# Performance work log

Hardware: AMD Instinct MI355X
Metric: run time of the kernel (lower is better)

Reference implementation:

```python
import jax, jax.numpy as jnp
import numpy as np

N_NODES = 100000
N_EDGES = 1600000
HIDDEN = 128
N_ETYPES = 4
N_STEPS = 4


def setup_inputs() -> dict:
    key = jax.random.key(0)
    ks = jax.random.split(key, 10)
    s = 1.0 / np.sqrt(HIDDEN)
    node_feat = jax.random.normal(ks[0], (N_NODES, HIDDEN), dtype=jnp.float32)
    edge_index = jax.random.randint(ks[1], (2, N_EDGES), 0, N_NODES)
    edge_feat = jax.random.uniform(ks[2], (N_EDGES, N_ETYPES), dtype=jnp.float32)
    # per-edge-type linear layers (DGL GatedGraphConv uses nn.Linear per etype)
    W_edge = jax.random.uniform(ks[3], (N_ETYPES, HIDDEN, HIDDEN), minval=-s, maxval=s, dtype=jnp.float32)
    b_edge = jax.random.uniform(ks[4], (N_ETYPES, HIDDEN), minval=-s, maxval=s, dtype=jnp.float32)
    # GRUCell parameters (torch layout: gates stacked r, z, n)
    W_ih = jax.random.uniform(ks[5], (3 * HIDDEN, HIDDEN), minval=-s, maxval=s, dtype=jnp.float32)
    W_hh = jax.random.uniform(ks[6], (3 * HIDDEN, HIDDEN), minval=-s, maxval=s, dtype=jnp.float32)
    b_ih = jax.random.uniform(ks[7], (3 * HIDDEN,), minval=-s, maxval=s, dtype=jnp.float32)
    b_hh = jax.random.uniform(ks[8], (3 * HIDDEN,), minval=-s, maxval=s, dtype=jnp.float32)
    return {"node_feat": node_feat, "edge_index": edge_index, "edge_feat": edge_feat,
            "W_edge": W_edge, "b_edge": b_edge, "W_ih": W_ih, "W_hh": W_hh,
            "b_ih": b_ih, "b_hh": b_hh}


def _gru_cell(x, h, W_ih, W_hh, b_ih, b_hh):
    gi = x @ W_ih.T + b_ih  # (N, 3D)
    gh = h @ W_hh.T + b_hh
    ir, iz, inn = jnp.split(gi, 3, axis=1)
    hr, hz, hn = jnp.split(gh, 3, axis=1)
    r = jax.nn.sigmoid(ir + hr)
    z = jax.nn.sigmoid(iz + hz)
    n = jnp.tanh(inn + r * hn)
    return (1.0 - z) * n + z * h


def reference(node_feat, edge_index, edge_feat, W_edge, b_edge, W_ih, W_hh, b_ih, b_hh):
    etypes = jnp.argmax(edge_feat, axis=1)          # (E,)
    src, dst = edge_index[0], edge_index[1]
    N = node_feat.shape[0]
    h = node_feat
    for _ in range(N_STEPS):
        # per-etype linear transform of all nodes: (T, N, D)
        trans = jnp.einsum('nd,tod->tno', h, W_edge) + b_edge[:, None, :]
        msg = trans[etypes, src]                    # (E, D) gather by (etype, src)
        a = jax.ops.segment_sum(msg, dst, num_segments=N)  # scatter-add to dst
        h = _gru_cell(a, h, W_ih, W_hh, b_ih, b_hh)
    return h
```

## Files before the change

kernel.cpp:

```cpp
#include <hip/hip_runtime.h>

#define N_NODES 100000
#define N_EDGES 1600000
#define HID 128
#define SCAN_N (N_NODES*4)
#define NB1 ((SCAN_N + 1023) / 1024)
#define ZERO_IDX (N_NODES*4)

#define EB 8192
#define NBLKA ((N_EDGES + EB - 1) / EB)
#define BSH 9
#define NBUCK ((N_NODES + (1<<BSH) - 1) >> BSH)
#define N2 (NBUCK * NBLKA)
#define NB2 ((N2 + 1023) / 1024)

typedef __attribute__((ext_vector_type(8))) short short8;
typedef __attribute__((ext_vector_type(4))) float float4v;
typedef __attribute__((ext_vector_type(4))) int int4v;
typedef __attribute__((ext_vector_type(2))) unsigned int uint2v;
typedef unsigned short ushort_t;
typedef unsigned int uint_t;

__device__ __forceinline__ float bits2f(uint_t u){ union{uint_t u; float f;} x; x.u=u; return x.f; }
__device__ __forceinline__ float b2f(ushort_t u){ return bits2f(((uint_t)u)<<16); }
__device__ __forceinline__ ushort_t f2b(float f){
  union{float f; uint_t u;} x; x.f=f;
  uint_t r = x.u + 0x7fffu + ((x.u>>16)&1u);
  return (ushort_t)(r>>16);
}
__device__ __forceinline__ float fsigm(float x){ return __builtin_amdgcn_rcpf(1.0f + __expf(-x)); }
__device__ __forceinline__ float ftanh(float x){ return 2.0f*__builtin_amdgcn_rcpf(1.0f + __expf(-2.0f*x)) - 1.0f; }
__device__ __forceinline__ float sigm(float x){ return 1.0f/(1.0f+__expf(-x)); }
__device__ __forceinline__ float tanh_f(float x){
  float t=__expf(-2.0f*fabsf(x)); float y=(1.0f-t)/(1.0f+t); return x>=0.f? y : -y;
}
__device__ __forceinline__ int imin(int a, int b){ return a < b ? a : b; }


__global__ void prep_weights(const float* __restrict__ W_edge, const float* __restrict__ W_ih,
                             const float* __restrict__ W_hh, ushort_t* __restrict__ WY,
                             ushort_t* __restrict__ W2f, ushort_t* __restrict__ WYf){
  int i = blockIdx.x*256 + threadIdx.x;
  if (i < 65536){
    WY[i] = f2b(W_edge[i]);
  } else if (i < 65536 + 131072){
    int i2 = i - 65536;
    int tile = i2 >> 9, e9 = i2 & 511;
    int lane = e9 >> 3, e = e9 & 7;
    int kk = tile & 1, kt = (tile >> 1) & 3, j = (tile >> 3) & 7, wn = tile >> 6;
    int lq = lane >> 4, l15 = lane & 15;
    int c = wn*32 + (j&1)*16 + l15;
    int jg = j >> 1;
    int k = kt*64 + (kk*4 + lq)*8 + e;
    float v;
    if (jg < 2)       v = (k < 128) ? W_ih[(jg*128 + c)*128 + k] : W_hh[(jg*128 + c)*128 + (k-128)];
    else if (jg == 2) v = (k < 128) ? W_ih[(256 + c)*128 + k] : 0.0f;
    else              v = (k >= 128) ? W_hh[(256 + c)*128 + (k-128)] : 0.0f;
    W2f[i2] = f2b(v);
  } else if (i < 65536 + 131072 + 65536){
    int i3 = i - 65536 - 131072;
    int tile = i3 >> 9, e9 = i3 & 511;
    int lane = e9 >> 3, e = e9 & 7;
    int kc = tile & 3, j = (tile >> 2) & 7, wn = tile >> 5;
    int lq = lane >> 4, l15 = lane & 15;
    int n = wn*128 + j*16 + l15;
    int k = kc*32 + lq*8 + e;
    WYf[i3] = f2b(W_edge[n*128 + k]);
  }
}

__global__ void edge_pass1(const int* __restrict__ eidx, const float* __restrict__ efeat,
                           int* __restrict__ packed, int* __restrict__ cnt,
                           int* __restrict__ bcntT){
  __shared__ int hist[NBUCK];
  int tid = threadIdx.x, blk = blockIdx.x;
  for (int j = tid; j < NBUCK; j += 512) hist[j] = 0;
  __syncthreads();
  #pragma unroll
  for (int k = 0; k < EB/512; ++k){
    int e = blk*EB + k*512 + tid;
    if (e < N_EDGES){
      int src = eidx[e], dst = eidx[N_EDGES + e];
      float4v f = *(const float4v*)(efeat + (size_t)e*4);
      int t = 0; float b = f[0];
      if (f[1] > b){ b = f[1]; t = 1; }
      if (f[2] > b){ b = f[2]; t = 2; }
      if (f[3] > b){ b = f[3]; t = 3; }
      packed[e] = (src << 2) | t;
      atomicAdd(&cnt[dst*4 + t], 1);
      atomicAdd(&hist[dst >> BSH], 1);
    }
  }
  __syncthreads();
  for (int j = tid; j < NBUCK; j += 512) bcntT[j*NBLKA + blk] = hist[j];
}

__global__ void scan_pass1(const int* __restrict__ src, int* __restrict__ bsum, int n){
  __shared__ int ws[4];
  int tid = threadIdx.x, lane = tid & 63, w = tid >> 6;
  int idx = blockIdx.x*1024 + tid*4;
  int v = 0;
  if (idx + 3 < n){ int4v x = *(const int4v*)(src + idx); v = x[0]+x[1]+x[2]+x[3]; }
  else { for (int k = 0; k < 4; ++k) if (idx + k < n) v += src[idx+k]; }
  for (int d = 32; d; d >>= 1) v += __shfl_down(v, d);
  if (lane == 0) ws[w] = v;
  __syncthreads();
  if (tid == 0) bsum[blockIdx.x] = ws[0]+ws[1]+ws[2]+ws[3];
}

__global__ void scan_pass2(const int* __restrict__ bsum, int* __restrict__ bpre,
                           int* __restrict__ total_out, int nb){
  __shared__ int sh[512];
  int tid = threadIdx.x;
  int v = (tid < nb) ? bsum[tid] : 0;
  sh[tid] = v;
  __syncthreads();
  for (int d = 1; d < 512; d <<= 1){
    int y = (tid >= d) ? sh[tid-d] : 0;
    __syncthreads();
    sh[tid] += y;
    __syncthreads();
  }
  if (tid < nb) bpre[tid] = sh[tid] - v;
  if (tid == 511) *total_out = sh[511];
}

__global__ void scan_pass3(const int* __restrict__ src, const int* __restrict__ bpre,
                           int* __restrict__ off, int n){
  __shared__ int wsum[4];
  int tid = threadIdx.x, lane = tid & 63, w = tid >> 6;
  int idx = blockIdx.x*1024 + tid*4;
  int v0=0,v1=0,v2=0,v3=0;
  if (idx + 3 < n){ int4v x = *(const int4v*)(src + idx); v0=x[0];v1=x[1];v2=x[2];v3=x[3]; }
  else {
    if (idx   < n) v0 = src[idx];
    if (idx+1 < n) v1 = src[idx+1];
    if (idx+2 < n) v2 = src[idx+2];
    if (idx+3 < n) v3 = src[idx+3];
  }
  int ts = v0+v1+v2+v3;
  int sc = ts;
  for (int d = 1; d < 64; d <<= 1){ int y = __shfl_up(sc, d); if (lane >= d) sc += y; }
  if (lane == 63) wsum[w] = sc;
  __syncthreads();
  int wofs = 0;
  for (int k = 0; k < w; ++k) wofs += wsum[k];
  int base = bpre[blockIdx.x] + wofs + sc - ts;
  int e0 = base, e1 = e0+v0, e2 = e1+v1, e3 = e2+v2;
  if (idx   < n) off[idx  ] = e0;
  if (idx+1 < n) off[idx+1] = e1;
  if (idx+2 < n) off[idx+2] = e2;
  if (idx+3 < n) off[idx+3] = e3;
}

__global__ void bucket_scatter(const int* __restrict__ eidx, const int* __restrict__ packed,
                               const int* __restrict__ boffT, int* __restrict__ bucketed){
  __shared__ int cur[NBUCK];
  int tid = threadIdx.x, blk = blockIdx.x;
  for (int j = tid; j < NBUCK; j += 512) cur[j] = boffT[j*NBLKA + blk];
  __syncthreads();
  #pragma unroll
  for (int k = 0; k < EB/512; ++k){
    int e = blk*EB + k*512 + tid;
    if (e < N_EDGES){
      int dst = eidx[N_EDGES + e];
      int pos = atomicAdd(&cur[dst >> BSH], 1);
      bucketed[pos] = ((dst & ((1<<BSH)-1)) << 19) | packed[e];
    }
  }
}

__global__ void bucket_sort(const int* __restrict__ bucketed, const int* __restrict__ boffT,
                            const int* __restrict__ off4, int* __restrict__ sorted){
  __shared__ int cur[(1<<BSH)*4];
  int tid = threadIdx.x, b = blockIdx.x;
  int base = b * ((1<<BSH)*4);
  for (int j = tid; j < (1<<BSH)*4; j += 512)
    cur[j] = off4[imin(base + j, SCAN_N)];
  __syncthreads();
  int s = boffT[b*NBLKA];
  int e = boffT[(b+1)*NBLKA];
  for (int i = s + tid; i < e; i += 512){
    int w = bucketed[i];
    int ci = ((w >> 19) << 2) | (w & 3);
    int pos = atomicAdd(&cur[ci], 1);
    sorted[pos] = w & 0x7FFFF;
  }
}

__global__ void init_h(const float* __restrict__ nf, ushort_t* __restrict__ hB, int n4){
  int i = blockIdx.x*256 + threadIdx.x;
  if (i >= n4) return;
  float4v v = *(const float4v*)(nf + (size_t)i*4);
  uint2v u;
  u[0] = (uint_t)f2b(v[0]) | ((uint_t)f2b(v[1])<<16);
  u[1] = (uint_t)f2b(v[2]) | ((uint_t)f2b(v[3])<<16);
  *(uint2v*)(hB + (size_t)i*4) = u;
}


__launch_bounds__(512, 2)
__global__ void transform_kernel(const ushort_t* __restrict__ hB, const ushort_t* __restrict__ WY,
                                 ushort_t* __restrict__ Y){
  __shared__ ushort_t lA[128*64];
  __shared__ ushort_t lB[512*64];
  int tid = threadIdx.x, w = tid >> 6, lane = tid & 63;
  int wm = w >> 2, wn = w & 3;
  int row0 = blockIdx.x * 128;
  float4v acc[4][8] = {};
  for (int kt = 0; kt < 2; ++kt){
    short8 va[2], vb[8];
    #pragma unroll
    for (int i = 0; i < 2; ++i){
      int cidx = i*512 + tid;
      int r = cidx >> 3, ch = cidx & 7;
      int node = row0 + r; if (node >= N_NODES) node = N_NODES-1;
      va[i] = *reinterpret_cast<const short8*>(hB + (size_t)node*128 + kt*64 + ch*8);
    }
    #pragma unroll
    for (int i = 0; i < 8; ++i){
      int cidx = i*512 + tid;
      int n = cidx >> 3, ch = cidx & 7;
      vb[i] = *reinterpret_cast<const short8*>(WY + (size_t)n*128 + kt*64 + ch*8);
    }
    __syncthreads();
    #pragma unroll
    for (int i = 0; i < 2; ++i){
      int cidx = i*512 + tid;
      int r = cidx >> 3, ch = cidx & 7;
      *reinterpret_cast<short8*>(lA + r*64 + ((ch ^ (r&7))<<3)) = va[i];
    }
    #pragma unroll
    for (int i = 0; i < 8; ++i){
      int cidx = i*512 + tid;
      int n = cidx >> 3, ch = cidx & 7;
      *reinterpret_cast<short8*>(lB + n*64 + ((ch ^ (n&7))<<3)) = vb[i];
    }
    __syncthreads();
    #pragma unroll
    for (int kk = 0; kk < 2; ++kk){
      int lch = kk*4 + (lane>>4);
      short8 af[4], bf[8];
      #pragma unroll
      for (int i = 0; i < 4; ++i){
        int r = wm*64 + i*16 + (lane&15);
        af[i] = *reinterpret_cast<const short8*>(lA + r*64 + ((lch ^ (r&7))<<3));
      }
      #pragma unroll
      for (int j = 0; j < 8; ++j){
        int n = wn*128 + j*16 + (lane&15);
        bf[j] = *reinterpret_cast<const short8*>(lB + n*64 + ((lch ^ (n&7))<<3));
      }
      #pragma unroll
      for (int i = 0; i < 4; ++i)
        #pragma unroll
        for (int j = 0; j < 8; ++j)
          acc[i][j] = __builtin_amdgcn_mfma_f32_16x16x32_bf16(af[i], bf[j], acc[i][j], 0, 0, 0);
    }
    __syncthreads();
  }
  #pragma unroll
  for (int i = 0; i < 4; ++i)
    #pragma unroll
    for (int j = 0; j < 8; ++j)
      #pragma unroll
      for (int q = 0; q < 4; ++q){
        int grow = row0 + wm*64 + i*16 + (lane>>4)*4 + q;
        if (grow >= N_NODES) continue;
        int colc = wn*128 + j*16 + (lane&15);
        Y[(size_t)grow*512 + colc] = f2b(acc[i][j][q]);
      }
}

__global__ void agg_kernel(const int* __restrict__ off4, const int* __restrict__ sorted,
                           const ushort_t* __restrict__ Y, const int* __restrict__ cnt,
                           const float* __restrict__ b_edge, ushort_t* __restrict__ aB){
  int wid = (int)((blockIdx.x * blockDim.x + threadIdx.x) >> 6);
  int lane = threadIdx.x & 63;
  if (wid >= N_NODES) return;
  int s = off4[wid*4], e = off4[wid*4+4];
  int col = lane*2;
  float p0=0,p1=0,q0=0,q1=0,r0=0,r1=0,t0=0,t1=0;
  for (int i = s; i < e; i += 16){
    int vv[16];
    #pragma unroll
    for (int k = 0; k < 16; ++k){
      int j = i + k;
      int sv = sorted[imin(j, e-1)];
      vv[k] = __builtin_amdgcn_readfirstlane(j < e ? sv : ZERO_IDX);
    }
    uint_t hv[16];
    #pragma unroll
    for (int k = 0; k < 16; ++k)
      hv[k] = *(const uint_t*)(Y + (size_t)vv[k]*128 + col);
    #pragma unroll
    for (int k = 0; k < 16; ++k){
      float f0 = bits2f((hv[k] & 0xffffu) << 16);
      float f1 = bits2f(hv[k] & 0xffff0000u);
      if ((k&3)==0){ p0+=f0; p1+=f1; }
      else if ((k&3)==1){ q0+=f0; q1+=f1; }
      else if ((k&3)==2){ r0+=f0; r1+=f1; }
      else { t0+=f0; t1+=f1; }
    }
  }
  float s0 = (p0+q0)+(r0+t0);
  float s1 = (p1+q1)+(r1+t1);
  int4v c4 = *(const int4v*)(cnt + wid*4);
  #pragma unroll
  for (int t = 0; t < 4; ++t){
    float cf = (float)c4[t];
    s0 += cf * b_edge[t*128 + col];
    s1 += cf * b_edge[t*128 + col + 1];
  }
  *(uint_t*)(aB + (size_t)wid*128 + col) = (uint_t)f2b(s0) | ((uint_t)f2b(s1) << 16);
}

__launch_bounds__(512, 4)
__global__ void gru_tr_kernel(const ushort_t* __restrict__ aB, ushort_t* __restrict__ hB,
                              const ushort_t* __restrict__ W2f, const ushort_t* __restrict__ WYf,
                              const float* __restrict__ b_ih, const float* __restrict__ b_hh,
                              float* __restrict__ hF, ushort_t* __restrict__ Y, int last){
  __shared__ ushort_t lA[2][4096];
  __shared__ ushort_t lH[8192];
  int tid = threadIdx.x, w = tid >> 6, lane = tid & 63;
  int wm = w >> 2, wn = w & 3;
  int l15 = lane & 15, lq = lane >> 4;
  int row0 = blockIdx.x * 64;

  int rS = tid >> 3, chS = tid & 7;
  int nodeS = imin(row0 + rS, N_NODES-1);
  size_t aoffS = (size_t)nodeS*128 + chS*8;
  int woS = rS*64 + ((chS ^ (rS&7))<<3);

  *reinterpret_cast<short8*>(&lA[0][woS]) = *reinterpret_cast<const short8*>(aB + aoffS);
  __syncthreads();

  float4v acc[2][8] = {};
  #pragma unroll
  for (int kt = 0; kt < 4; ++kt){
    short8 vn = {};
    if (kt < 3){
      const ushort_t* srcN = (kt+1 < 2) ? aB : hB;
      vn = *reinterpret_cast<const short8*>(srcN + aoffS + ((kt+1)&1)*64);
    }
    bool lo = (kt < 2);
    const ushort_t* lcur = lA[kt&1];
    #pragma unroll
    for (int kk = 0; kk < 2; ++kk){
      int lch = kk*4 + lq;
      short8 af[2];
      #pragma unroll
      for (int i = 0; i < 2; ++i){
        int r = wm*32 + i*16 + l15;
        af[i] = *reinterpret_cast<const short8*>(lcur + r*64 + ((lch ^ (r&7))<<3));
      }
      #pragma unroll
      for (int j = 0; j < 8; ++j){
        if (lo ? (j >= 6) : (j == 4 || j == 5)) continue;
        int tile = ((wn*8 + j)*4 + kt)*2 + kk;
        short8 bf = *reinterpret_cast<const short8*>(W2f + (size_t)tile*512 + lane*8);
        #pragma unroll
        for (int i = 0; i < 2; ++i)
          acc[i][j] = __builtin_amdgcn_mfma_f32_16x16x32_bf16(af[i], bf, acc[i][j], 0, 0, 0);
      }
    }
    if (kt < 3)
      *reinterpret_cast<short8*>(&lA[(kt+1)&1][woS]) = vn;
    __syncthreads();
  }
  #pragma unroll
  for (int i = 0; i < 2; ++i){
    #pragma unroll
    for (int jj = 0; jj < 2; ++jj){
      int c = wn*32 + jj*16 + l15;
      float bir = b_ih[c] + b_hh[c];
      float biz = b_ih[128+c] + b_hh[128+c];
      float bni = b_ih[256+c], bnh = b_hh[256+c];
      int cl = c & 63;
      const ushort_t* lh = lA[c >> 6];
      int ch = c >> 3;
      #pragma unroll
      for (int q = 0; q < 4; ++q){
        int row = wm*32 + i*16 + lq*4 + q;
        float rg = fsigm(acc[i][0+jj][q] + bir);
        float zg = fsigm(acc[i][2+jj][q] + biz);
        float hn = acc[i][6+jj][q] + bnh;
        float nn = ftanh(acc[i][4+jj][q] + bni + rg*hn);
        float h = b2f(lh[row*64 + (((cl>>3) ^ (row&7))<<3) + (cl&7)]);
        float out = (1.0f - zg)*nn + zg*h;
        lH[row*128 + ((ch ^ (row&15))<<3) + (c&7)] = f2b(out);
      }
    }
  }
  __syncthreads();
  #pragma unroll
  for (int p = 0; p < 2; ++p){
    int u = p*512 + tid;
    int row = u >> 4, uc = u & 15;
    int grow = row0 + row;
    if (grow < N_NODES){
      short8 v = *reinterpret_cast<const short8*>(lH + row*128 + ((uc ^ (row&15))<<3));
      *reinterpret_cast<short8*>(hB + (size_t)grow*128 + uc*8) = v;
      if (last){
        float4v f0, f1;
        #pragma unroll
        for (int k = 0; k < 4; ++k) f0[k] = b2f((ushort_t)v[k]);
        #pragma unroll
        for (int k = 0; k < 4; ++k) f1[k] = b2f((ushort_t)v[4+k]);
        *reinterpret_cast<float4v*>(hF + (size_t)grow*128 + uc*8)     = f0;
        *reinterpret_cast<float4v*>(hF + (size_t)grow*128 + uc*8 + 4) = f1;
      }
    }
  }
  if (last) return;
  float4v acc2[2][8] = {};
  #pragma unroll
  for (int kc = 0; kc < 4; ++kc){
    int lchh = kc*4 + lq;
    short8 af[2];
    #pragma unroll
    for (int i = 0; i < 2; ++i){
      int r = wm*32 + i*16 + l15;
      af[i] = *reinterpret_cast<const short8*>(lH + r*128 + ((lchh ^ (r&15))<<3));
    }
    #pragma unroll
    for (int j = 0; j < 8; ++j){
      int tile = (wn*8 + j)*4 + kc;
      short8 bf = *reinterpret_cast<const short8*>(WYf + (size_t)tile*512 + lane*8);
      #pragma unroll
      for (int i = 0; i < 2; ++i)
        acc2[i][j] = __builtin_amdgcn_mfma_f32_16x16x32_bf16(af[i], bf, acc2[i][j], 0, 0, 0);
    }
  }
  #pragma unroll
  for (int i = 0; i < 2; ++i)
    #pragma unroll
    for (int q = 0; q < 4; ++q){
      int grow = row0 + wm*32 + i*16 + lq*4 + q;
      if (grow >= N_NODES) continue;
      #pragma unroll
      for (int j = 0; j < 8; ++j)
        Y[(size_t)grow*512 + wn*128 + j*16 + l15] = f2b(acc2[i][q == 0 ? j : j][q]);
    }
}


extern "C" void kernel_launch(void* const* d_in, const int* in_sizes, int n_in,
                              void* d_out, int out_size, void* d_ws, size_t ws_size,
                              hipStream_t stream) {
  const float* node_feat = (const float*)d_in[0];
  const int*   edge_idx  = (const int*)d_in[1];
  const float* edge_feat = (const float*)d_in[2];
  const float* W_edge    = (const float*)d_in[3];
  const float* b_edge    = (const float*)d_in[4];
  const float* W_ih      = (const float*)d_in[5];
  const float* W_hh      = (const float*)d_in[6];
  const float* b_ih      = (const float*)d_in[7];
  const float* b_hh      = (const float*)d_in[8];
  float* hF = (float*)d_out;

  char* p = (char*)d_ws;
  auto take = [&](size_t bytes) -> char* {
    char* r = p; p += (bytes + 255) & ~(size_t)255; return r;
  };
  ushort_t* WY     = (ushort_t*)take(512*128*2);
  ushort_t* W2f    = (ushort_t*)take(131072*2);
  ushort_t* WYf    = (ushort_t*)take(65536*2);
  int* cnt      = (int*)take((size_t)SCAN_N*4);
  int* off4     = (int*)take((size_t)(SCAN_N+1)*4);
  int* bcntT    = (int*)take((size_t)N2*4);
  int* boffT    = (int*)take((size_t)(N2+1)*4);
  int* bsum     = (int*)take(512*4);
  int* bpre     = (int*)take(512*4);
  int* packed   = (int*)take((size_t)N_EDGES*4);
  int* bucketed = (int*)take((size_t)N_EDGES*4);
  int* sorted   = (int*)take((size_t)N_EDGES*4);
  ushort_t* hB = (ushort_t*)take((size_t)N_NODES*128*2);
  ushort_t* Y  = (ushort_t*)take(((size_t)N_NODES*512 + 256)*2);
  ushort_t* aB = (ushort_t*)take((size_t)N_NODES*128*2);

  hipMemsetAsync(cnt, 0, (size_t)SCAN_N*4, stream);
  hipMemsetAsync(Y + (size_t)N_NODES*512, 0, 256*2, stream);

  prep_weights<<<1024, 256, 0, stream>>>(W_edge, W_ih, W_hh, WY, W2f, WYf);
  edge_pass1<<<NBLKA, 512, 0, stream>>>(edge_idx, edge_feat, packed, cnt, bcntT);
  scan_pass1<<<NB1, 256, 0, stream>>>(cnt, bsum, SCAN_N);
  scan_pass2<<<1, 512, 0, stream>>>(bsum, bpre, off4 + SCAN_N, NB1);
  scan_pass3<<<NB1, 256, 0, stream>>>(cnt, bpre, off4, SCAN_N);
  scan_pass1<<<NB2, 256, 0, stream>>>(bcntT, bsum, N2);
  scan_pass2<<<1, 512, 0, stream>>>(bsum, bpre, boffT + N2, NB2);
  scan_pass3<<<NB2, 256, 0, stream>>>(bcntT, bpre, boffT, N2);
  bucket_scatter<<<NBLKA, 512, 0, stream>>>(edge_idx, packed, boffT, bucketed);
  bucket_sort<<<NBUCK, 512, 0, stream>>>(bucketed, boffT, off4, sorted);
  init_h<<<(N_NODES*32 + 255)/256, 256, 0, stream>>>(node_feat, hB, N_NODES*32);

  int gb = (N_NODES + 127) / 128;
  int gb2 = (N_NODES + 63) / 64;
  transform_kernel<<<gb, 512, 0, stream>>>(hB, WY, Y);
  for (int step = 0; step < 4; ++step){
    agg_kernel<<<(N_NODES+3)/4, 256, 0, stream>>>(off4, sorted, Y, cnt, b_edge, aB);
    gru_tr_kernel<<<gb2, 512, 0, stream>>>(aB, hB, W2f, WYf, b_ih, b_hh, hF, Y, step == 3);
  }
}
```

Baseline: 759.0 us.

## Permute hidden-feature order so MFMA epilogues emit packed vector stores

Hidden features are stored everywhere in a permuted order (pinv) chosen so each lane's MFMA accumulator columns are contiguous. Transform and GRU epilogues can then pack eight outputs with v_cvt_pk_bf16_f32 into one 16-byte store instead of scattered 2-byte stores. Weights, biases and the initial state are permuted once in the prep and init kernels. The cost is that the final fp32 output is un-permuted with strided scalar stores, and init_h now does scattered reads.

```diff
diff --git a/kernel.cpp b/kernel.cpp
--- a/kernel.cpp
+++ b/kernel.cpp
@@ -17,6 +17,7 @@
 typedef __attribute__((ext_vector_type(8))) short short8;
 typedef __attribute__((ext_vector_type(4))) float float4v;
 typedef __attribute__((ext_vector_type(4))) int int4v;
+typedef __attribute__((ext_vector_type(4))) unsigned int uint4v;
 typedef __attribute__((ext_vector_type(2))) unsigned int uint2v;
 typedef unsigned short ushort_t;
 typedef unsigned int uint_t;
@@ -28,21 +29,23 @@
   uint_t r = x.u + 0x7fffu + ((x.u>>16)&1u);
   return (ushort_t)(r>>16);
 }
+__device__ __forceinline__ uint_t cvtpk(float a, float b){
+  uint_t r; asm("v_cvt_pk_bf16_f32 %0, %1, %2" : "=v"(r) : "v"(a), "v"(b)); return r;
+}
 __device__ __forceinline__ float fsigm(float x){ return __builtin_amdgcn_rcpf(1.0f + __expf(-x)); }
 __device__ __forceinline__ float ftanh(float x){ return 2.0f*__builtin_amdgcn_rcpf(1.0f + __expf(-2.0f*x)) - 1.0f; }
-__device__ __forceinline__ float sigm(float x){ return 1.0f/(1.0f+__expf(-x)); }
-__device__ __forceinline__ float tanh_f(float x){
-  float t=__expf(-2.0f*fabsf(x)); float y=(1.0f-t)/(1.0f+t); return x>=0.f? y : -y;
-}
 __device__ __forceinline__ int imin(int a, int b){ return a < b ? a : b; }
+__device__ __forceinline__ int pinv(int p){ return ((p&7)<<4) | (p>>3); }
 
 
 __global__ void prep_weights(const float* __restrict__ W_edge, const float* __restrict__ W_ih,
-                             const float* __restrict__ W_hh, ushort_t* __restrict__ WY,
-                             ushort_t* __restrict__ W2f, ushort_t* __restrict__ WYf){
+                             const float* __restrict__ W_hh, const float* __restrict__ b_edge,
+                             ushort_t* __restrict__ WY, ushort_t* __restrict__ W2f,
+                             ushort_t* __restrict__ WYf, float* __restrict__ bEp){
   int i = blockIdx.x*256 + threadIdx.x;
   if (i < 65536){
-    WY[i] = f2b(W_edge[i]);
+    int g = i >> 7, p = i & 127;
+    WY[i] = f2b(W_edge[g*128 + pinv(p)]);
   } else if (i < 65536 + 131072){
     int i2 = i - 65536;
     int tile = i2 >> 9, e9 = i2 & 511;
@@ -52,10 +55,12 @@
     int c = wn*32 + (j&1)*16 + l15;
     int jg = j >> 1;
     int k = kt*64 + (kk*4 + lq)*8 + e;
+    int d = pinv(k & 127);
+    bool aside = (k < 128);
     float v;
-    if (jg < 2)       v = (k < 128) ? W_ih[(jg*128 + c)*128 + k] : W_hh[(jg*128 + c)*128 + (k-128)];
-    else if (jg == 2) v = (k < 128) ? W_ih[(256 + c)*128 + k] : 0.0f;
-    else              v = (k >= 128) ? W_hh[(256 + c)*128 + (k-128)] : 0.0f;
+    if (jg < 2)       v = aside ? W_ih[(jg*128 + c)*128 + d] : W_hh[(jg*128 + c)*128 + d];
+    else if (jg == 2) v = aside ? W_ih[(256 + c)*128 + d] : 0.0f;
+    else              v = aside ? 0.0f : W_hh[(256 + c)*128 + d];
     W2f[i2] = f2b(v);
   } else if (i < 65536 + 131072 + 65536){
     int i3 = i - 65536 - 131072;
@@ -65,7 +70,11 @@
     int lq = lane >> 4, l15 = lane & 15;
     int n = wn*128 + j*16 + l15;
     int k = kc*32 + lq*8 + e;
-    WYf[i3] = f2b(W_edge[n*128 + k]);
+    WYf[i3] = f2b(W_edge[n*128 + pinv(k)]);
+  } else if (i < 65536 + 131072 + 65536 + 512){
+    int i4 = i - 65536 - 131072 - 65536;
+    int t = i4 >> 7, p = i4 & 127;
+    bEp[i4] = b_edge[t*128 + pinv(p)];
   }
 }
 
@@ -188,14 +197,13 @@
   }
 }
 
-__global__ void init_h(const float* __restrict__ nf, ushort_t* __restrict__ hB, int n4){
+__global__ void init_h(const float* __restrict__ nf, ushort_t* __restrict__ hB, int n){
   int i = blockIdx.x*256 + threadIdx.x;
-  if (i >= n4) return;
-  float4v v = *(const float4v*)(nf + (size_t)i*4);
-  uint2v u;
-  u[0] = (uint_t)f2b(v[0]) | ((uint_t)f2b(v[1])<<16);
-  u[1] = (uint_t)f2b(v[2]) | ((uint_t)f2b(v[3])<<16);
-  *(uint2v*)(hB + (size_t)i*4) = u;
+  if (i >= n) return;
+  int v = i >> 6, pp = (i & 63)*2;
+  float f0 = nf[(size_t)v*128 + pinv(pp)];
+  float f1 = nf[(size_t)v*128 + pinv(pp+1)];
+  *(uint_t*)(hB + (size_t)v*128 + pp) = (uint_t)f2b(f0) | ((uint_t)f2b(f1)<<16);
 }
 
 
@@ -259,22 +267,25 @@
     }
     __syncthreads();
   }
+  int l15 = lane & 15;
   #pragma unroll
   for (int i = 0; i < 4; ++i)
     #pragma unroll
-    for (int j = 0; j < 8; ++j)
-      #pragma unroll
-      for (int q = 0; q < 4; ++q){
-        int grow = row0 + wm*64 + i*16 + (lane>>4)*4 + q;
-        if (grow >= N_NODES) continue;
-        int colc = wn*128 + j*16 + (lane&15);
-        Y[(size_t)grow*512 + colc] = f2b(acc[i][j][q]);
-      }
+    for (int q = 0; q < 4; ++q){
+      int grow = row0 + wm*64 + i*16 + (lane>>4)*4 + q;
+      if (grow >= N_NODES) continue;
+      uint4v u;
+      u[0] = cvtpk(acc[i][0][q], acc[i][1][q]);
+      u[1] = cvtpk(acc[i][2][q], acc[i][3][q]);
+      u[2] = cvtpk(acc[i][4][q], acc[i][5][q]);
+      u[3] = cvtpk(acc[i][6][q], acc[i][7][q]);
+      *reinterpret_cast<uint4v*>(Y + (size_t)grow*512 + wn*128 + l15*8) = u;
+    }
 }
 
 __global__ void agg_kernel(const int* __restrict__ off4, const int* __restrict__ sorted,
                            const ushort_t* __restrict__ Y, const int* __restrict__ cnt,
-                           const float* __restrict__ b_edge, ushort_t* __restrict__ aB){
+                           const float* __restrict__ bEp, ushort_t* __restrict__ aB){
   int wid = (int)((blockIdx.x * blockDim.x + threadIdx.x) >> 6);
   int lane = threadIdx.x & 63;
   if (wid >= N_NODES) return;
@@ -309,8 +320,8 @@
   #pragma unroll
   for (int t = 0; t < 4; ++t){
     float cf = (float)c4[t];
-    s0 += cf * b_edge[t*128 + col];
-    s1 += cf * b_edge[t*128 + col + 1];
+    s0 += cf * bEp[t*128 + col];
+    s1 += cf * bEp[t*128 + col + 1];
   }
   *(uint_t*)(aB + (size_t)wid*128 + col) = (uint_t)f2b(s0) | ((uint_t)f2b(s1) << 16);
 }
@@ -368,27 +379,32 @@
       *reinterpret_cast<short8*>(&lA[(kt+1)&1][woS]) = vn;
     __syncthreads();
   }
-  #pragma unroll
-  for (int i = 0; i < 2; ++i){
-    #pragma unroll
-    for (int jj = 0; jj < 2; ++jj){
-      int c = wn*32 + jj*16 + l15;
-      float bir = b_ih[c] + b_hh[c];
-      float biz = b_ih[128+c] + b_hh[128+c];
-      float bni = b_ih[256+c], bnh = b_hh[256+c];
-      int cl = c & 63;
-      const ushort_t* lh = lA[c >> 6];
-      int ch = c >> 3;
+  {
+    int c0 = wn*32 + l15, c1 = c0 + 16;
+    float bir0 = b_ih[c0] + b_hh[c0],       bir1 = b_ih[c1] + b_hh[c1];
+    float biz0 = b_ih[128+c0] + b_hh[128+c0], biz1 = b_ih[128+c1] + b_hh[128+c1];
+    float bni0 = b_ih[256+c0], bni1 = b_ih[256+c1];
+    float bnh0 = b_hh[256+c0], bnh1 = b_hh[256+c1];
+    int sc = l15*8 + wn*2;
+    const ushort_t* lhh = lA[sc >> 6];
+    int scl = sc & 63;
+    #pragma unroll
+    for (int i = 0; i < 2; ++i){
       #pragma unroll
       for (int q = 0; q < 4; ++q){
         int row = wm*32 + i*16 + lq*4 + q;
-        float rg = fsigm(acc[i][0+jj][q] + bir);
-        float zg = fsigm(acc[i][2+jj][q] + biz);
-        float hn = acc[i][6+jj][q] + bnh;
-        float nn = ftanh(acc[i][4+jj][q] + bni + rg*hn);
-        float h = b2f(lh[row*64 + (((cl>>3) ^ (row&7))<<3) + (cl&7)]);
-        float out = (1.0f - zg)*nn + zg*h;
-        lH[row*128 + ((ch ^ (row&15))<<3) + (c&7)] = f2b(out);
+        uint_t hu = *(const uint_t*)(lhh + row*64 + (((scl>>3) ^ (row&7))<<3) + (scl&7));
+        float h0 = bits2f((hu & 0xffffu) << 16);
+        float h1 = bits2f(hu & 0xffff0000u);
+        float rg0 = fsigm(acc[i][0][q] + bir0);
+        float zg0 = fsigm(acc[i][2][q] + biz0);
+        float nn0 = ftanh(acc[i][4][q] + bni0 + rg0*(acc[i][6][q] + bnh0));
+        float out0 = (1.0f - zg0)*nn0 + zg0*h0;
+        float rg1 = fsigm(acc[i][1][q] + bir1);
+        float zg1 = fsigm(acc[i][3][q] + biz1);
+        float nn1 = ftanh(acc[i][5][q] + bni1 + rg1*(acc[i][7][q] + bnh1));
+        float out1 = (1.0f - zg1)*nn1 + zg1*h1;
+        *(uint_t*)(lH + row*128 + ((l15 ^ (row&15))<<3) + wn*2) = cvtpk(out0, out1);
       }
     }
   }
@@ -402,13 +418,9 @@
       short8 v = *reinterpret_cast<const short8*>(lH + row*128 + ((uc ^ (row&15))<<3));
       *reinterpret_cast<short8*>(hB + (size_t)grow*128 + uc*8) = v;
       if (last){
-        float4v f0, f1;
         #pragma unroll
-        for (int k = 0; k < 4; ++k) f0[k] = b2f((ushort_t)v[k]);
-        #pragma unroll
-        for (int k = 0; k < 4; ++k) f1[k] = b2f((ushort_t)v[4+k]);
-        *reinterpret_cast<float4v*>(hF + (size_t)grow*128 + uc*8)     = f0;
-        *reinterpret_cast<float4v*>(hF + (size_t)grow*128 + uc*8 + 4) = f1;
+        for (int s = 0; s < 8; ++s)
+          hF[(size_t)grow*128 + s*16 + uc] = b2f((ushort_t)v[s]);
       }
     }
   }
@@ -438,9 +450,12 @@
     for (int q = 0; q < 4; ++q){
       int grow = row0 + wm*32 + i*16 + lq*4 + q;
       if (grow >= N_NODES) continue;
-      #pragma unroll
-      for (int j = 0; j < 8; ++j)
-        Y[(size_t)grow*512 + wn*128 + j*16 + l15] = f2b(acc2[i][q == 0 ? j : j][q]);
+      uint4v u;
+      u[0] = cvtpk(acc2[i][0][q], acc2[i][1][q]);
+      u[1] = cvtpk(acc2[i][2][q], acc2[i][3][q]);
+      u[2] = cvtpk(acc2[i][4][q], acc2[i][5][q]);
+      u[3] = cvtpk(acc2[i][6][q], acc2[i][7][q]);
+      *reinterpret_cast<uint4v*>(Y + (size_t)grow*512 + wn*128 + l15*8) = u;
     }
 }
 
@@ -466,6 +481,7 @@
   ushort_t* WY     = (ushort_t*)take(512*128*2);
   ushort_t* W2f    = (ushort_t*)take(131072*2);
   ushort_t* WYf    = (ushort_t*)take(65536*2);
+  float*    bEp    = (float*)take(512*4);
   int* cnt      = (int*)take((size_t)SCAN_N*4);
   int* off4     = (int*)take((size_t)(SCAN_N+1)*4);
   int* bcntT    = (int*)take((size_t)N2*4);
@@ -482,7 +498,7 @@
   hipMemsetAsync(cnt, 0, (size_t)SCAN_N*4, stream);
   hipMemsetAsync(Y + (size_t)N_NODES*512, 0, 256*2, stream);
 
-  prep_weights<<<1024, 256, 0, stream>>>(W_edge, W_ih, W_hh, WY, W2f, WYf);
+  prep_weights<<<1028, 256, 0, stream>>>(W_edge, W_ih, W_hh, b_edge, WY, W2f, WYf, bEp);
   edge_pass1<<<NBLKA, 512, 0, stream>>>(edge_idx, edge_feat, packed, cnt, bcntT);
   scan_pass1<<<NB1, 256, 0, stream>>>(cnt, bsum, SCAN_N);
   scan_pass2<<<1, 512, 0, stream>>>(bsum, bpre, off4 + SCAN_N, NB1);
@@ -492,13 +508,13 @@
   scan_pass3<<<NB2, 256, 0, stream>>>(bcntT, bpre, boffT, N2);
   bucket_scatter<<<NBLKA, 512, 0, stream>>>(edge_idx, packed, boffT, bucketed);
   bucket_sort<<<NBUCK, 512, 0, stream>>>(bucketed, boffT, off4, sorted);
-  init_h<<<(N_NODES*32 + 255)/256, 256, 0, stream>>>(node_feat, hB, N_NODES*32);
+  init_h<<<(N_NODES*64 + 255)/256, 256, 0, stream>>>(node_feat, hB, N_NODES*64);
 
   int gb = (N_NODES + 127) / 128;
   int gb2 = (N_NODES + 63) / 64;
   transform_kernel<<<gb, 512, 0, stream>>>(hB, WY, Y);
   for (int step = 0; step < 4; ++step){
-    agg_kernel<<<(N_NODES+3)/4, 256, 0, stream>>>(off4, sorted, Y, cnt, b_edge, aB);
+    agg_kernel<<<(N_NODES+3)/4, 256, 0, stream>>>(off4, sorted, Y, cnt, bEp, aB);
     gru_tr_kernel<<<gb2, 512, 0, stream>>>(aB, hB, W2f, WYf, b_ih, b_hh, hF, Y, step == 3);
   }
 }
```

Result: faster. 707.6 us (median of 2 runs) (-6.8%).
